# Optimization experiments

Hardware: AMD Instinct MI355X
Metric: run time of the kernel (lower is better)

Reference implementation:

```python
import jax, jax.numpy as jnp
import numpy as np

B, T, K = 32, 8192, 16
EPS = 1e-7
LAM_FIRE, LAM_CANCEL, LAM_VALID, LAM_WRITE = 1.0, 1.0, 0.5, 0.5


def setup_inputs() -> dict:
    key = jax.random.key(0)
    ks = jax.random.split(key, 11)
    return {
        "trigger_hazard": jax.random.uniform(ks[0], (B, T, K), jnp.float32),
        "validity": jax.random.uniform(ks[1], (B, T, K), jnp.float32),
        "cancel_logits": jax.random.normal(ks[2], (B, T, K, 3), jnp.float32),
        "write_score": jax.random.normal(ks[3], (B, T, 1), jnp.float32),
        "live_mask": jax.random.randint(ks[4], (B, T, K), 0, 2).astype(bool),
        "contract_id": jax.random.randint(ks[5], (B, T, K), 0, 32),
        "oracle_fire": jax.random.randint(ks[6], (B, T, K), 0, 2).astype(jnp.float32),
        "oracle_cancel": jax.random.randint(ks[7], (B, T, K), 0, 4),
        "oracle_valid": jax.random.randint(ks[8], (B, T, K), 0, 2).astype(jnp.float32),
        "oracle_should_write": jax.random.randint(ks[9], (B, T, 1), 0, 2).astype(jnp.float32),
        "oracle_contract_id": jax.random.randint(ks[10], (B, T, K), 0, 32),
    }


def _masked_bce(p_raw, y, m):
    # Mirrors torch: BCE(clamp(p)*mask, y*mask), then *mask, sum / clamp(mask.sum(),1)
    n = jnp.maximum(m.sum(), 1.0)
    p = jnp.clip(p_raw, EPS, 1.0 - EPS) * m
    t = y * m
    # extra inner clip only guards masked entries (p==0), which are zeroed anyway
    bce = -(t * jnp.log(jnp.clip(p, EPS)) + (1.0 - t) * jnp.log(jnp.clip(1.0 - p, EPS)))
    return (bce * m).sum() / n


def _cancel_ce(logits, cancel_tgt, live_mask):
    has = ((cancel_tgt > 0) & live_mask).astype(jnp.float32)  # (B,T,K)
    n = has.sum()
    tgt = jnp.clip(cancel_tgt - 1, 0).astype(jnp.int32)
    logp = jax.nn.log_softmax(logits, axis=-1)  # (B,T,K,3)
    ce = -jnp.take_along_axis(logp, tgt[..., None], axis=-1)[..., 0]
    return jnp.where(n > 0, (ce * has).sum() / jnp.maximum(n, 1.0), 0.0)


def _bce_with_logits(x, y):
    return jnp.mean(jnp.maximum(x, 0.0) - x * y + jnp.log1p(jnp.exp(-jnp.abs(x))))


def reference(trigger_hazard, validity, cancel_logits, write_score, live_mask,
              contract_id, oracle_fire, oracle_cancel, oracle_valid,
              oracle_should_write, oracle_contract_id):
    # Vectorized align_oracle_to_model: broadcast compare + first-match argmax + gather
    match = (contract_id[..., :, None] == oracle_contract_id[..., None, :]) \
            & (contract_id != 0)[..., None]              # (B,T,Km,Ko)
    found = match.any(axis=-1)                           # (B,T,Km)
    idx = jnp.argmax(match, axis=-1)                     # first matching oracle slot

    def align_f(x):  # float tensors -> zeros where unmatched (torch out = zeros float)
        return jnp.where(found, jnp.take_along_axis(x, idx, axis=2), 0.0)

    fire_t = align_f(oracle_fire)
    valid_t = align_f(oracle_valid)
    cancel_t = jnp.where(found, jnp.take_along_axis(oracle_cancel, idx, axis=2), 0)

    m = live_mask.astype(jnp.float32)
    fire = LAM_FIRE * _masked_bce(trigger_hazard, fire_t, m)
    cancel = LAM_CANCEL * _cancel_ce(cancel_logits, cancel_t, live_mask)
    valid = LAM_VALID * _masked_bce(validity, valid_t, m)
    write = LAM_WRITE * _bce_with_logits(write_score, oracle_should_write)
    total = fire + cancel + valid + write
    return jnp.stack([fire, cancel, valid, write, total])
```

## Files before the change

kernel.cpp:

```cpp
#include <hip/hip_runtime.h>
#include <math.h>

#define EPS_F 1e-7f

constexpr int Bc = 32, Tc = 8192, Kc = 16;
constexpr int ROWS   = Bc * Tc;
constexpr int BLOCK  = 256;
constexpr int NITEM4 = ROWS * 4;
constexpr int NTILE  = NITEM4 / BLOCK;
constexpr int NBLK   = 512;
constexpr int TPB    = NTILE / NBLK;

constexpr int W_OCID = 0;
constexpr int W_OCAN = 1024;
constexpr int W_OFIR = 2048;
constexpr int W_OVAL = 3072;
constexpr int W_CID  = 4096;
constexpr int W_LIVE = 5120;
constexpr int W_TRIG = 6144;
constexpr int W_VALP = 7168;
constexpr int W_CLOG = 8192;
constexpr int W_WSC  = 11264;
constexpr int W_OSW  = 11520;
constexpr int BUFB   = 11776;
constexpr int DEPTH  = 2;
constexpr int SMEM_BYTES = 4 * DEPTH * BUFB;

typedef unsigned long long u64;

__device__ __forceinline__ u64 shflx64(u64 v, int m) {
  unsigned lo = __shfl_xor((unsigned)v, m, 64);
  unsigned hi = __shfl_xor((unsigned)(v >> 32), m, 64);
  return ((u64)hi << 32) | lo;
}

__device__ __forceinline__ void dma16(void* lds, const void* g) {
  __builtin_amdgcn_global_load_lds(
      (const __attribute__((address_space(1))) void*)g,
      (__attribute__((address_space(3))) void*)lds, 16, 0, 0);
}
__device__ __forceinline__ void dma4(void* lds, const void* g) {
  __builtin_amdgcn_global_load_lds(
      (const __attribute__((address_space(1))) void*)g,
      (__attribute__((address_space(3))) void*)lds, 4, 0, 0);
}

#define WAITCNT_VM(N)                                                      \
  do {                                                                     \
    asm volatile("s_waitcnt vmcnt(" #N ")" ::: "memory");                  \
    __builtin_amdgcn_sched_barrier(0);                                     \
  } while (0)

__device__ __forceinline__ void stage_tile(
    char* sb, int gt, int w, int lane,
    const char* trig, const char* valp, const char* clog, const char* wscore,
    const char* live, const char* cid, const char* ofire, const char* ocan,
    const char* ovalid, const char* oshw, const char* ocid)
{
  const size_t o16 = (size_t)(gt * 256 + w * 64 + lane) * 16;
  dma16(sb + W_OCID, ocid   + o16);
  dma16(sb + W_OCAN, ocan   + o16);
  dma16(sb + W_OFIR, ofire  + o16);
  dma16(sb + W_OVAL, ovalid + o16);
  dma16(sb + W_CID,  cid    + o16);
  dma16(sb + W_LIVE, live   + o16);
  dma16(sb + W_TRIG, trig   + o16);
  dma16(sb + W_VALP, valp   + o16);
  const char* gc = clog + (size_t)(gt * 256 + w * 64) * 48;
  dma16(sb + W_CLOG + 0,    gc + 0    + lane * 16);
  dma16(sb + W_CLOG + 1024, gc + 1024 + lane * 16);
  dma16(sb + W_CLOG + 2048, gc + 2048 + lane * 16);
  const size_t ro = (size_t)(gt * 64 + lane) * 4;
  dma4(sb + W_WSC, wscore + ro);
  dma4(sb + W_OSW, oshw   + ro);
}

__global__ __launch_bounds__(BLOCK) void loss_main(
    const float* __restrict__ trig,
    const float* __restrict__ valp,
    const float* __restrict__ clog,
    const float* __restrict__ wscore,
    const int*   __restrict__ live,
    const int*   __restrict__ cid,
    const float* __restrict__ ofire,
    const int*   __restrict__ ocan,
    const float* __restrict__ ovalid,
    const float* __restrict__ oshw,
    const int*   __restrict__ ocid,
    float* __restrict__ part)
{
  __shared__ __align__(16) char smem[SMEM_BYTES];

  const int tid  = threadIdx.x;
  const int lane = tid & 63;
  const int w    = tid >> 6;
  const int gt0  = blockIdx.x * TPB;

  const char* trig_b   = (const char*)trig;
  const char* valp_b   = (const char*)valp;
  const char* clog_b   = (const char*)clog;
  const char* wscore_b = (const char*)wscore;
  const char* live_b   = (const char*)live;
  const char* cid_b    = (const char*)cid;
  const char* ofire_b  = (const char*)ofire;
  const char* ocan_b   = (const char*)ocan;
  const char* ovalid_b = (const char*)ovalid;
  const char* oshw_b   = (const char*)oshw;
  const char* ocid_b   = (const char*)ocid;

  char* wb = smem + (size_t)w * (DEPTH * BUFB);

  stage_tile(wb, gt0, w, lane, trig_b, valp_b, clog_b, wscore_b, live_b,
             cid_b, ofire_b, ocan_b, ovalid_b, oshw_b, ocid_b);

  float a0 = 0.f, a1 = 0.f, a2 = 0.f, a3 = 0.f, a4 = 0.f, a5 = 0.f;

  for (int t = 0; t < TPB; ++t) {
    char* sb = wb + (t & 1) * BUFB;

    if (t + 1 < TPB) {
      asm volatile("s_waitcnt lgkmcnt(0)" ::: "memory");
      stage_tile(wb + ((t + 1) & 1) * BUFB, gt0 + t + 1, w, lane,
                 trig_b, valp_b, clog_b, wscore_b, live_b, cid_b,
                 ofire_b, ocan_b, ovalid_b, oshw_b, ocid_b);
      WAITCNT_VM(13);
    } else {
      WAITCNT_VM(0);
    }

    const int4   oc = *(const int4*)  (sb + W_OCID + lane * 16);
    const int4   cc = *(const int4*)  (sb + W_OCAN + lane * 16);
    const float4 ff = *(const float4*)(sb + W_OFIR + lane * 16);
    const float4 vv = *(const float4*)(sb + W_OVAL + lane * 16);
    const int4   cd = *(const int4*)  (sb + W_CID  + lane * 16);
    const int4   lm = *(const int4*)  (sb + W_LIVE + lane * 16);
    const float4 ph = *(const float4*)(sb + W_TRIG + lane * 16);
    const float4 pq = *(const float4*)(sb + W_VALP + lane * 16);
    const float4 lA = *(const float4*)(sb + W_CLOG + lane * 48 + 0);
    const float4 lB = *(const float4*)(sb + W_CLOG + lane * 48 + 16);
    const float4 lC = *(const float4*)(sb + W_CLOG + lane * 48 + 32);
    const float  wx = *(const float*) (sb + W_WSC + (tid >> 2) * 4);
    const float  wy = *(const float*) (sb + W_OSW + (tid >> 2) * 4);

    u64 tblLo = 0ull, tblHi = 0ull, fndLo = 0ull, fndHi = 0ull;
    {
      const int   ocs[4] = {oc.x, oc.y, oc.z, oc.w};
      const int   ccs[4] = {cc.x, cc.y, cc.z, cc.w};
      const float ffs[4] = {ff.x, ff.y, ff.z, ff.w};
      const float vvs[4] = {vv.x, vv.y, vv.z, vv.w};
      #pragma unroll
      for (int j = 0; j < 4; ++j) {
        const unsigned c  = (unsigned)ocs[j] & 31u;
        const unsigned sh = (c & 15u) * 4u;
        const bool isLo   = c < 16u;
        const bool seen   = (((isLo ? fndLo : fndHi) >> sh) & 1ull) != 0ull;
        const unsigned nib = (unsigned)ffs[j] | ((unsigned)vvs[j] << 1) |
                             ((unsigned)ccs[j] << 2);
        const u64 add  = seen ? 0ull : ((u64)nib << sh);
        const u64 fadd = 0xFull << sh;
        tblLo |= isLo ? add : 0ull;
        tblHi |= isLo ? 0ull : add;
        fndLo |= isLo ? fadd : 0ull;
        fndHi |= isLo ? 0ull : fadd;
      }
    }

    #pragma unroll
    for (int m = 1; m <= 2; m <<= 1) {
      const u64 pTL = shflx64(tblLo, m);
      const u64 pTH = shflx64(tblHi, m);
      const u64 pFL = shflx64(fndLo, m);
      const u64 pFH = shflx64(fndHi, m);
      const bool iLow = (lane & m) == 0;
      const u64 loTL = iLow ? tblLo : pTL, hiTL = iLow ? pTL : tblLo;
      const u64 loTH = iLow ? tblHi : pTH, hiTH = iLow ? pTH : tblHi;
      const u64 loFL = iLow ? fndLo : pFL, hiFL = iLow ? pFL : fndLo;
      const u64 loFH = iLow ? fndHi : pFH, hiFH = iLow ? pFH : fndHi;
      tblLo = loTL | (hiTL & ~loFL);
      tblHi = loTH | (hiTH & ~loFH);
      fndLo = loFL | hiFL;
      fndHi = loFH | hiFH;
    }

    {
      const int   cds[4] = {cd.x, cd.y, cd.z, cd.w};
      const int   lms[4] = {lm.x, lm.y, lm.z, lm.w};
      const float phs[4] = {ph.x, ph.y, ph.z, ph.w};
      const float pqs[4] = {pq.x, pq.y, pq.z, pq.w};
      const float L0[4] = {lA.x, lA.w, lB.z, lC.y};
      const float L1[4] = {lA.y, lB.x, lB.w, lC.z};
      const float L2[4] = {lA.z, lB.y, lC.x, lC.w};
      #pragma unroll
      for (int j = 0; j < 4; ++j) {
        const unsigned c  = (unsigned)cds[j] & 31u;
        const unsigned sh = (c & 15u) * 4u;
        const bool isLo   = c < 16u;
        const bool fnd = (c != 0u) &&
                         ((((isLo ? fndLo : fndHi) >> sh) & 1ull) != 0ull);
        unsigned nib = (unsigned)(((isLo ? tblLo : tblHi) >> sh)) & 15u;
        nib = fnd ? nib : 0u;
        const float fire_t = (float)(nib & 1u);
        const float val_t  = (float)((nib >> 1) & 1u);
        const int   can_t  = (int)(nib >> 2);

        const float m = lms[j] ? 1.f : 0.f;

        const float p  = fminf(fmaxf(phs[j], EPS_F), 1.f - EPS_F);
        const float bf = -__logf((fire_t != 0.f) ? p : 1.f - p);
        const float q  = fminf(fmaxf(pqs[j], EPS_F), 1.f - EPS_F);
        const float bv = -__logf((val_t != 0.f) ? q : 1.f - q);

        const float has = (can_t > 0 && lms[j]) ? 1.f : 0.f;
        const int tgt = (can_t - 1) < 0 ? 0 : (can_t - 1);
        const float l0 = L0[j], l1 = L1[j], l2 = L2[j];
        const float mx  = fmaxf(l0, fmaxf(l1, l2));
        const float lse = mx + __logf(__expf(l0 - mx) + __expf(l1 - mx) +
                                      __expf(l2 - mx));
        const float lt  = (tgt == 0) ? l0 : ((tgt == 1) ? l1 : l2);

        a0 += bf * m;
        a1 += m;
        a2 += (lse - lt) * has;
        a3 += has;
        a4 += bv * m;
      }
    }

    if ((tid & 3) == 0) {
      a5 += fmaxf(wx, 0.f) - wx * wy + __logf(1.f + __expf(-fabsf(wx)));
    }
  }

  float v[6] = {a0, a1, a2, a3, a4, a5};
  #pragma unroll
  for (int off = 32; off > 0; off >>= 1) {
    #pragma unroll
    for (int i = 0; i < 6; ++i) v[i] += __shfl_down(v[i], off, 64);
  }
  __shared__ float red[4][6];
  if (lane == 0) {
    #pragma unroll
    for (int i = 0; i < 6; ++i) red[w][i] = v[i];
  }
  __syncthreads();
  if (tid == 0) {
    #pragma unroll
    for (int i = 0; i < 6; ++i)
      part[blockIdx.x * 6 + i] = red[0][i] + red[1][i] + red[2][i] + red[3][i];
  }
}

__global__ __launch_bounds__(BLOCK) void loss_finalize(
    const float* __restrict__ part, float* __restrict__ out)
{
  double v[6] = {0, 0, 0, 0, 0, 0};
  for (int r = threadIdx.x; r < NBLK; r += BLOCK) {
    #pragma unroll
    for (int i = 0; i < 6; ++i) v[i] += (double)part[r * 6 + i];
  }
  #pragma unroll
  for (int off = 32; off > 0; off >>= 1) {
    #pragma unroll
    for (int i = 0; i < 6; ++i) v[i] += __shfl_down(v[i], off, 64);
  }
  __shared__ double red[4][6];
  const int w = threadIdx.x >> 6, lane = threadIdx.x & 63;
  if (lane == 0) {
    #pragma unroll
    for (int i = 0; i < 6; ++i) red[w][i] = v[i];
  }
  __syncthreads();
  if (threadIdx.x == 0) {
    double a[6];
    #pragma unroll
    for (int i = 0; i < 6; ++i) a[i] = red[0][i] + red[1][i] + red[2][i] + red[3][i];
    const double live_n = a[1] < 1.0 ? 1.0 : a[1];
    const double fire   = a[0] / live_n;
    const double cancel = (a[3] > 0.0) ? a[2] / (a[3] < 1.0 ? 1.0 : a[3])
                                       : 0.0;
    const double valid  = 0.5 * a[4] / live_n;
    const double wr     = 0.5 * a[5] / (double)ROWS;
    out[0] = (float)fire;
    out[1] = (float)cancel;
    out[2] = (float)valid;
    out[3] = (float)wr;
    out[4] = (float)(fire + cancel + valid + wr);
  }
}

extern "C" void kernel_launch(void* const* d_in, const int* in_sizes, int n_in,
                              void* d_out, int out_size, void* d_ws, size_t ws_size,
                              hipStream_t stream) {
  const float* trig   = (const float*)d_in[0];
  const float* valp   = (const float*)d_in[1];
  const float* clog   = (const float*)d_in[2];
  const float* wscore = (const float*)d_in[3];
  const int*   live   = (const int*)  d_in[4];
  const int*   cid    = (const int*)  d_in[5];
  const float* ofire  = (const float*)d_in[6];
  const int*   ocan   = (const int*)  d_in[7];
  const float* ovalid = (const float*)d_in[8];
  const float* oshw   = (const float*)d_in[9];
  const int*   ocid   = (const int*)  d_in[10];
  float* out  = (float*)d_out;
  float* part = (float*)d_ws;

  loss_main<<<NBLK, BLOCK, 0, stream>>>(trig, valp, clog, wscore, live, cid,
                                        ofire, ocan, ovalid, oshw, ocid, part);
  loss_finalize<<<1, BLOCK, 0, stream>>>(part, out);
}
```

Measured before the change: 215.0 us.

## Replace LDS double-buffered DMA pipeline with direct global loads, one tile per block

```diff
diff --git a/kernel.cpp b/kernel.cpp
--- a/kernel.cpp
+++ b/kernel.cpp
@@ -7,24 +7,7 @@
 constexpr int ROWS   = Bc * Tc;
 constexpr int BLOCK  = 256;
 constexpr int NITEM4 = ROWS * 4;
-constexpr int NTILE  = NITEM4 / BLOCK;
-constexpr int NBLK   = 512;
-constexpr int TPB    = NTILE / NBLK;
-
-constexpr int W_OCID = 0;
-constexpr int W_OCAN = 1024;
-constexpr int W_OFIR = 2048;
-constexpr int W_OVAL = 3072;
-constexpr int W_CID  = 4096;
-constexpr int W_LIVE = 5120;
-constexpr int W_TRIG = 6144;
-constexpr int W_VALP = 7168;
-constexpr int W_CLOG = 8192;
-constexpr int W_WSC  = 11264;
-constexpr int W_OSW  = 11520;
-constexpr int BUFB   = 11776;
-constexpr int DEPTH  = 2;
-constexpr int SMEM_BYTES = 4 * DEPTH * BUFB;
+constexpr int NBLK   = NITEM4 / BLOCK;
 
 typedef unsigned long long u64;
 
@@ -32,47 +15,6 @@
   unsigned lo = __shfl_xor((unsigned)v, m, 64);
   unsigned hi = __shfl_xor((unsigned)(v >> 32), m, 64);
   return ((u64)hi << 32) | lo;
-}
-
-__device__ __forceinline__ void dma16(void* lds, const void* g) {
-  __builtin_amdgcn_global_load_lds(
-      (const __attribute__((address_space(1))) void*)g,
-      (__attribute__((address_space(3))) void*)lds, 16, 0, 0);
-}
-__device__ __forceinline__ void dma4(void* lds, const void* g) {
-  __builtin_amdgcn_global_load_lds(
-      (const __attribute__((address_space(1))) void*)g,
-      (__attribute__((address_space(3))) void*)lds, 4, 0, 0);
-}
-
-#define WAITCNT_VM(N)                                                      \
-  do {                                                                     \
-    asm volatile("s_waitcnt vmcnt(" #N ")" ::: "memory");                  \
-    __builtin_amdgcn_sched_barrier(0);                                     \
-  } while (0)
-
-__device__ __forceinline__ void stage_tile(
-    char* sb, int gt, int w, int lane,
-    const char* trig, const char* valp, const char* clog, const char* wscore,
-    const char* live, const char* cid, const char* ofire, const char* ocan,
-    const char* ovalid, const char* oshw, const char* ocid)
-{
-  const size_t o16 = (size_t)(gt * 256 + w * 64 + lane) * 16;
-  dma16(sb + W_OCID, ocid   + o16);
-  dma16(sb + W_OCAN, ocan   + o16);
-  dma16(sb + W_OFIR, ofire  + o16);
-  dma16(sb + W_OVAL, ovalid + o16);
-  dma16(sb + W_CID,  cid    + o16);
-  dma16(sb + W_LIVE, live   + o16);
-  dma16(sb + W_TRIG, trig   + o16);
-  dma16(sb + W_VALP, valp   + o16);
-  const char* gc = clog + (size_t)(gt * 256 + w * 64) * 48;
-  dma16(sb + W_CLOG + 0,    gc + 0    + lane * 16);
-  dma16(sb + W_CLOG + 1024, gc + 1024 + lane * 16);
-  dma16(sb + W_CLOG + 2048, gc + 2048 + lane * 16);
-  const size_t ro = (size_t)(gt * 64 + lane) * 4;
-  dma4(sb + W_WSC, wscore + ro);
-  dma4(sb + W_OSW, oshw   + ro);
 }
 
 __global__ __launch_bounds__(BLOCK) void loss_main(
@@ -89,146 +31,115 @@
     const int*   __restrict__ ocid,
     float* __restrict__ part)
 {
-  __shared__ __align__(16) char smem[SMEM_BYTES];
-
   const int tid  = threadIdx.x;
   const int lane = tid & 63;
-  const int w    = tid >> 6;
-  const int gt0  = blockIdx.x * TPB;
-
-  const char* trig_b   = (const char*)trig;
-  const char* valp_b   = (const char*)valp;
-  const char* clog_b   = (const char*)clog;
-  const char* wscore_b = (const char*)wscore;
-  const char* live_b   = (const char*)live;
-  const char* cid_b    = (const char*)cid;
-  const char* ofire_b  = (const char*)ofire;
-  const char* ocan_b   = (const char*)ocan;
-  const char* ovalid_b = (const char*)ovalid;
-  const char* oshw_b   = (const char*)oshw;
-  const char* ocid_b   = (const char*)ocid;
-
-  char* wb = smem + (size_t)w * (DEPTH * BUFB);
-
-  stage_tile(wb, gt0, w, lane, trig_b, valp_b, clog_b, wscore_b, live_b,
-             cid_b, ofire_b, ocan_b, ovalid_b, oshw_b, ocid_b);
-
-  float a0 = 0.f, a1 = 0.f, a2 = 0.f, a3 = 0.f, a4 = 0.f, a5 = 0.f;
-
-  for (int t = 0; t < TPB; ++t) {
-    char* sb = wb + (t & 1) * BUFB;
-
-    if (t + 1 < TPB) {
-      asm volatile("s_waitcnt lgkmcnt(0)" ::: "memory");
-      stage_tile(wb + ((t + 1) & 1) * BUFB, gt0 + t + 1, w, lane,
-                 trig_b, valp_b, clog_b, wscore_b, live_b, cid_b,
-                 ofire_b, ocan_b, ovalid_b, oshw_b, ocid_b);
-      WAITCNT_VM(13);
-    } else {
-      WAITCNT_VM(0);
+  const int gi   = blockIdx.x * BLOCK + tid;
+  const size_t o16 = (size_t)gi * 16;
+  const size_t o48 = (size_t)gi * 48;
+
+  const int4   oc = *(const int4*)  ((const char*)ocid   + o16);
+  const int4   cc = *(const int4*)  ((const char*)ocan   + o16);
+  const float4 ff = *(const float4*)((const char*)ofire  + o16);
+  const float4 vv = *(const float4*)((const char*)ovalid + o16);
+  const int4   cd = *(const int4*)  ((const char*)cid    + o16);
+  const int4   lm = *(const int4*)  ((const char*)live   + o16);
+  const float4 ph = *(const float4*)((const char*)trig   + o16);
+  const float4 pq = *(const float4*)((const char*)valp   + o16);
+  const float4 lA = *(const float4*)((const char*)clog   + o48 + 0);
+  const float4 lB = *(const float4*)((const char*)clog   + o48 + 16);
+  const float4 lC = *(const float4*)((const char*)clog   + o48 + 32);
+  const int row = gi >> 2;
+  const float wx = wscore[row];
+  const float wy = oshw[row];
+
+  u64 tblLo = 0ull, tblHi = 0ull, fndLo = 0ull, fndHi = 0ull;
+  {
+    const int   ocs[4] = {oc.x, oc.y, oc.z, oc.w};
+    const int   ccs[4] = {cc.x, cc.y, cc.z, cc.w};
+    const float ffs[4] = {ff.x, ff.y, ff.z, ff.w};
+    const float vvs[4] = {vv.x, vv.y, vv.z, vv.w};
+    #pragma unroll
+    for (int j = 0; j < 4; ++j) {
+      const unsigned c  = (unsigned)ocs[j] & 31u;
+      const unsigned sh = (c & 15u) * 4u;
+      const bool isLo   = c < 16u;
+      const bool seen   = (((isLo ? fndLo : fndHi) >> sh) & 1ull) != 0ull;
+      const unsigned nib = (unsigned)ffs[j] | ((unsigned)vvs[j] << 1) |
+                           ((unsigned)ccs[j] << 2);
+      const u64 add  = seen ? 0ull : ((u64)nib << sh);
+      const u64 fadd = 0xFull << sh;
+      tblLo |= isLo ? add : 0ull;
+      tblHi |= isLo ? 0ull : add;
+      fndLo |= isLo ? fadd : 0ull;
+      fndHi |= isLo ? 0ull : fadd;
     }
-
-    const int4   oc = *(const int4*)  (sb + W_OCID + lane * 16);
-    const int4   cc = *(const int4*)  (sb + W_OCAN + lane * 16);
-    const float4 ff = *(const float4*)(sb + W_OFIR + lane * 16);
-    const float4 vv = *(const float4*)(sb + W_OVAL + lane * 16);
-    const int4   cd = *(const int4*)  (sb + W_CID  + lane * 16);
-    const int4   lm = *(const int4*)  (sb + W_LIVE + lane * 16);
-    const float4 ph = *(const float4*)(sb + W_TRIG + lane * 16);
-    const float4 pq = *(const float4*)(sb + W_VALP + lane * 16);
-    const float4 lA = *(const float4*)(sb + W_CLOG + lane * 48 + 0);
-    const float4 lB = *(const float4*)(sb + W_CLOG + lane * 48 + 16);
-    const float4 lC = *(const float4*)(sb + W_CLOG + lane * 48 + 32);
-    const float  wx = *(const float*) (sb + W_WSC + (tid >> 2) * 4);
-    const float  wy = *(const float*) (sb + W_OSW + (tid >> 2) * 4);
-
-    u64 tblLo = 0ull, tblHi = 0ull, fndLo = 0ull, fndHi = 0ull;
-    {
-      const int   ocs[4] = {oc.x, oc.y, oc.z, oc.w};
-      const int   ccs[4] = {cc.x, cc.y, cc.z, cc.w};
-      const float ffs[4] = {ff.x, ff.y, ff.z, ff.w};
-      const float vvs[4] = {vv.x, vv.y, vv.z, vv.w};
-      #pragma unroll
-      for (int j = 0; j < 4; ++j) {
-        const unsigned c  = (unsigned)ocs[j] & 31u;
-        const unsigned sh = (c & 15u) * 4u;
-        const bool isLo   = c < 16u;
-        const bool seen   = (((isLo ? fndLo : fndHi) >> sh) & 1ull) != 0ull;
-        const unsigned nib = (unsigned)ffs[j] | ((unsigned)vvs[j] << 1) |
-                             ((unsigned)ccs[j] << 2);
-        const u64 add  = seen ? 0ull : ((u64)nib << sh);
-        const u64 fadd = 0xFull << sh;
-        tblLo |= isLo ? add : 0ull;
-        tblHi |= isLo ? 0ull : add;
-        fndLo |= isLo ? fadd : 0ull;
-        fndHi |= isLo ? 0ull : fadd;
-      }
+  }
+
+  #pragma unroll
+  for (int m = 1; m <= 2; m <<= 1) {
+    const u64 pTL = shflx64(tblLo, m);
+    const u64 pTH = shflx64(tblHi, m);
+    const u64 pFL = shflx64(fndLo, m);
+    const u64 pFH = shflx64(fndHi, m);
+    const bool iLow = (lane & m) == 0;
+    const u64 loTL = iLow ? tblLo : pTL, hiTL = iLow ? pTL : tblLo;
+    const u64 loTH = iLow ? tblHi : pTH, hiTH = iLow ? pTH : tblHi;
+    const u64 loFL = iLow ? fndLo : pFL, hiFL = iLow ? pFL : fndLo;
+    const u64 loFH = iLow ? fndHi : pFH, hiFH = iLow ? pFH : fndHi;
+    tblLo = loTL | (hiTL & ~loFL);
+    tblHi = loTH | (hiTH & ~loFH);
+    fndLo = loFL | hiFL;
+    fndHi = loFH | hiFH;
+  }
+
+  float a0 = 0.f, a1 = 0.f, a2 = 0.f, a3 = 0.f, a4 = 0.f;
+  {
+    const int   cds[4] = {cd.x, cd.y, cd.z, cd.w};
+    const int   lms[4] = {lm.x, lm.y, lm.z, lm.w};
+    const float phs[4] = {ph.x, ph.y, ph.z, ph.w};
+    const float pqs[4] = {pq.x, pq.y, pq.z, pq.w};
+    const float L0[4] = {lA.x, lA.w, lB.z, lC.y};
+    const float L1[4] = {lA.y, lB.x, lB.w, lC.z};
+    const float L2[4] = {lA.z, lB.y, lC.x, lC.w};
+    #pragma unroll
+    for (int j = 0; j < 4; ++j) {
+      const unsigned c  = (unsigned)cds[j] & 31u;
+      const unsigned sh = (c & 15u) * 4u;
+      const bool isLo   = c < 16u;
+      const bool fnd = (c != 0u) &&
+                       ((((isLo ? fndLo : fndHi) >> sh) & 1ull) != 0ull);
+      unsigned nib = (unsigned)(((isLo ? tblLo : tblHi) >> sh)) & 15u;
+      nib = fnd ? nib : 0u;
+      const float fire_t = (float)(nib & 1u);
+      const float val_t  = (float)((nib >> 1) & 1u);
+      const int   can_t  = (int)(nib >> 2);
+
+      const float m = lms[j] ? 1.f : 0.f;
+
+      const float p  = fminf(fmaxf(phs[j], EPS_F), 1.f - EPS_F);
+      const float bf = -__logf((fire_t != 0.f) ? p : 1.f - p);
+      const float q  = fminf(fmaxf(pqs[j], EPS_F), 1.f - EPS_F);
+      const float bv = -__logf((val_t != 0.f) ? q : 1.f - q);
+
+      const float has = (can_t > 0 && lms[j]) ? 1.f : 0.f;
+      const int tgt = (can_t - 1) < 0 ? 0 : (can_t - 1);
+      const float l0 = L0[j], l1 = L1[j], l2 = L2[j];
+      const float mx  = fmaxf(l0, fmaxf(l1, l2));
+      const float lse = mx + __logf(__expf(l0 - mx) + __expf(l1 - mx) +
+                                    __expf(l2 - mx));
+      const float lt  = (tgt == 0) ? l0 : ((tgt == 1) ? l1 : l2);
+
+      a0 += bf * m;
+      a1 += m;
+      a2 += (lse - lt) * has;
+      a3 += has;
+      a4 += bv * m;
     }
-
-    #pragma unroll
-    for (int m = 1; m <= 2; m <<= 1) {
-      const u64 pTL = shflx64(tblLo, m);
-      const u64 pTH = shflx64(tblHi, m);
-      const u64 pFL = shflx64(fndLo, m);
-      const u64 pFH = shflx64(fndHi, m);
-      const bool iLow = (lane & m) == 0;
-      const u64 loTL = iLow ? tblLo : pTL, hiTL = iLow ? pTL : tblLo;
-      const u64 loTH = iLow ? tblHi : pTH, hiTH = iLow ? pTH : tblHi;
-      const u64 loFL = iLow ? fndLo : pFL, hiFL = iLow ? pFL : fndLo;
-      const u64 loFH = iLow ? fndHi : pFH, hiFH = iLow ? pFH : fndHi;
-      tblLo = loTL | (hiTL & ~loFL);
-      tblHi = loTH | (hiTH & ~loFH);
-      fndLo = loFL | hiFL;
-      fndHi = loFH | hiFH;
-    }
-
-    {
-      const int   cds[4] = {cd.x, cd.y, cd.z, cd.w};
-      const int   lms[4] = {lm.x, lm.y, lm.z, lm.w};
-      const float phs[4] = {ph.x, ph.y, ph.z, ph.w};
-      const float pqs[4] = {pq.x, pq.y, pq.z, pq.w};
-      const float L0[4] = {lA.x, lA.w, lB.z, lC.y};
-      const float L1[4] = {lA.y, lB.x, lB.w, lC.z};
-      const float L2[4] = {lA.z, lB.y, lC.x, lC.w};
-      #pragma unroll
-      for (int j = 0; j < 4; ++j) {
-        const unsigned c  = (unsigned)cds[j] & 31u;
-        const unsigned sh = (c & 15u) * 4u;
-        const bool isLo   = c < 16u;
-        const bool fnd = (c != 0u) &&
-                         ((((isLo ? fndLo : fndHi) >> sh) & 1ull) != 0ull);
-        unsigned nib = (unsigned)(((isLo ? tblLo : tblHi) >> sh)) & 15u;
-        nib = fnd ? nib : 0u;
-        const float fire_t = (float)(nib & 1u);
-        const float val_t  = (float)((nib >> 1) & 1u);
-        const int   can_t  = (int)(nib >> 2);
-
-        const float m = lms[j] ? 1.f : 0.f;
-
-        const float p  = fminf(fmaxf(phs[j], EPS_F), 1.f - EPS_F);
-        const float bf = -__logf((fire_t != 0.f) ? p : 1.f - p);
-        const float q  = fminf(fmaxf(pqs[j], EPS_F), 1.f - EPS_F);
-        const float bv = -__logf((val_t != 0.f) ? q : 1.f - q);
-
-        const float has = (can_t > 0 && lms[j]) ? 1.f : 0.f;
-        const int tgt = (can_t - 1) < 0 ? 0 : (can_t - 1);
-        const float l0 = L0[j], l1 = L1[j], l2 = L2[j];
-        const float mx  = fmaxf(l0, fmaxf(l1, l2));
-        const float lse = mx + __logf(__expf(l0 - mx) + __expf(l1 - mx) +
-                                      __expf(l2 - mx));
-        const float lt  = (tgt == 0) ? l0 : ((tgt == 1) ? l1 : l2);
-
-        a0 += bf * m;
-        a1 += m;
-        a2 += (lse - lt) * has;
-        a3 += has;
-        a4 += bv * m;
-      }
-    }
-
-    if ((tid & 3) == 0) {
-      a5 += fmaxf(wx, 0.f) - wx * wy + __logf(1.f + __expf(-fabsf(wx)));
-    }
+  }
+
+  float a5 = 0.f;
+  if ((tid & 3) == 0) {
+    a5 = fmaxf(wx, 0.f) - wx * wy + __logf(1.f + __expf(-fabsf(wx)));
   }
 
   float v[6] = {a0, a1, a2, a3, a4, a5};
@@ -238,6 +149,7 @@
     for (int i = 0; i < 6; ++i) v[i] += __shfl_down(v[i], off, 64);
   }
   __shared__ float red[4][6];
+  const int w = tid >> 6;
   if (lane == 0) {
     #pragma unroll
     for (int i = 0; i < 6; ++i) red[w][i] = v[i];
```

Measured after the change: 212.1 us. No clear change (-1.3%).
